# Performance work log

Measured on AMD Instinct MI355X. Metric: run time of the kernel, lower is better.

Reference implementation:

```python
import jax, jax.numpy as jnp
import numpy as np

TARGET_KAPPA = 1.0 / 61.0
EPS = 1e-10

# --- antisymmetric expansion: 35 independent components (i<j<k) -> (7,7,7) ---
_combos = np.array([(i, j, k) for i in range(7) for j in range(i + 1, 7) for k in range(j + 1, 7)])  # (35,3)
_perm_specs = [((0, 1, 2), 1.0), ((0, 2, 1), -1.0), ((1, 0, 2), -1.0), ((1, 2, 0), 1.0), ((2, 0, 1), 1.0), ((2, 1, 0), -1.0)]
_I = jnp.array(np.concatenate([_combos[:, p[0]] for p, _ in _perm_specs]))
_J = jnp.array(np.concatenate([_combos[:, p[1]] for p, _ in _perm_specs]))
_K = jnp.array(np.concatenate([_combos[:, p[2]] for p, _ in _perm_specs]))
_S = jnp.array(np.concatenate([np.full(35, s, dtype=np.float32) for _, s in _perm_specs]))


def expand_to_antisymmetric(v35):
    # v35: (35,) -> antisymmetric (7,7,7)
    vals = jnp.tile(v35, 6) * _S.astype(v35.dtype)
    return jnp.zeros((7, 7, 7), v35.dtype).at[_I, _J, _K].set(vals)


def _phi_single(xi, W1, b1, W2, b2):
    # xi: (7,) -> antisymmetric 3-form (7,7,7)
    h = jnp.tanh(xi @ W1 + b1)          # (H,)
    v35 = h @ W2 + b2                    # (35,)
    return expand_to_antisymmetric(v35)


def setup_inputs() -> dict:
    key = jax.random.key(0)
    k1, k2, k3 = jax.random.split(key, 3)
    B, H = 32768, 512
    x = jax.random.normal(k1, (B, 7), dtype=jnp.float32)
    W1 = jax.random.normal(k2, (7, H), dtype=jnp.float32) * 0.3
    b1 = jnp.zeros((H,), dtype=jnp.float32)
    W2 = jax.random.normal(k3, (H, 35), dtype=jnp.float32) * 0.05
    b2 = jnp.zeros((35,), dtype=jnp.float32)
    return {"x": x, "W1": W1, "b1": b1, "W2": W2, "b2": b2}


def reference(x, W1, b1, W2, b2):
    f = lambda xi: _phi_single(xi, W1, b1, W2, b2)
    # Jacobian replaces the 35 looped autograd.grad calls: (B,7,7,7,7), last axis = d/dx_l
    jac = jax.vmap(jax.jacfwd(f))(x)
    d_phi = jnp.moveaxis(jac, -1, 1)  # (B, 7(deriv), 7, 7, 7), matching torch layout
    torsion_sq = jnp.sum(d_phi ** 2, axis=(1, 2, 3, 4))  # (B,)
    torsion_norm = jnp.sqrt(torsion_sq + EPS)
    loss = jnp.mean((torsion_norm - TARGET_KAPPA) ** 2)
    return loss, jnp.mean(torsion_norm)
```

## Files before the change

### kernel.cpp

```cpp
#include <hip/hip_runtime.h>
#include <hip/hip_bf16.h>
#include <math.h>

typedef __attribute__((ext_vector_type(8)))  short bf16x8;
typedef __attribute__((ext_vector_type(16))) float f32x16;
typedef unsigned int u32;

#define KAPPA (1.0f/61.0f)
#define NBLK 512

__device__ __forceinline__ unsigned short f2bf(float f) {
    u32 x = __float_as_uint(f);
    x += 0x7fffu + ((x >> 16) & 1u);
    return (unsigned short)(x >> 16);
}
__device__ __forceinline__ float fast_rcp(float v) {
#if __has_builtin(__builtin_amdgcn_rcpf)
    return __builtin_amdgcn_rcpf(v);
#else
    return 1.0f / v;
#endif
}
__device__ __forceinline__ u32 pack_bf16(float lo, float hi) {
    __hip_bfloat162 p = __float22bfloat162_rn(make_float2(lo, hi));
    return *reinterpret_cast<u32*>(&p);
}

__global__ void build_v(const float* __restrict__ W1, const float* __restrict__ W2,
                        const float* __restrict__ b1,
                        bf16x8* __restrict__ V, bf16x8* __restrict__ Wt) {
    int t = blockIdx.x * blockDim.x + threadIdx.x;
    if (t < 16384) {
        int lane = t & 63, ptile = (t >> 6) & 7, kkg = t >> 9;
        int p  = ptile * 32 + (lane & 31);
        int hb = kkg * 16 + (lane >> 5) * 8;
        bool valid = (p < 245);
        int l7 = valid ? p / 35 : 0;
        int c  = valid ? p - l7 * 35 : 0;
        bf16x8 v;
#pragma unroll
        for (int i = 0; i < 8; ++i) {
            int h = hb + i;
            v[i] = valid ? (short)f2bf(W1[l7 * 512 + h] * W2[h * 35 + c]) : (short)0;
        }
        V[t] = v;
    } else if (t < 16384 + 1024) {
        int f = t - 16384;
        int lane = f & 63, htile = f >> 6;
        int h = htile * 32 + (lane & 31);
        bf16x8 v;
#pragma unroll
        for (int i = 0; i < 8; ++i) v[i] = 0;
        if (lane < 32) {
#pragma unroll
            for (int l = 0; l < 7; ++l) v[l] = (short)f2bf(W1[l * 512 + h]);
            v[7] = (short)f2bf(b1[h]);
        }
        Wt[f] = v;
    }
}

__global__ __launch_bounds__(256, 3)
void torsion_main(const float* __restrict__ x,
                  const bf16x8* __restrict__ V, const bf16x8* __restrict__ Wt,
                  float* __restrict__ partials) {
    __shared__ __align__(16) u32 Gb[2][8][64 * 4];
    __shared__ float red[4][2][32];

    const int tid  = threadIdx.x;
    const int lane = tid & 63;
    const int w    = tid >> 6;
    const int blk  = blockIdx.x;
    const int rt   = w & 1;
    const int ht   = w >> 1;

    bf16x8 xf;
#pragma unroll
    for (int i = 0; i < 8; ++i) xf[i] = 0;
    if (lane < 32) {
        const float* xp = x + ((size_t)blk * 64 + rt * 32 + lane) * 7;
#pragma unroll
        for (int l = 0; l < 7; ++l) xf[l] = (short)f2bf(xp[l]);
        xf[7] = (short)f2bf(1.0f);
    }

    f32x16 acc[2][2];
#pragma unroll
    for (int pt = 0; pt < 2; ++pt)
#pragma unroll
        for (int r2 = 0; r2 < 2; ++r2)
#pragma unroll
            for (int e = 0; e < 16; ++e) acc[pt][r2][e] = 0.0f;

    auto pre_pack = [&](int c, u32 d[8]) {
        bf16x8 wf = Wt[(c * 2 + ht) * 64 + lane];
        f32x16 p;
#pragma unroll
        for (int e = 0; e < 16; ++e) p[e] = 0.0f;
        p = __builtin_amdgcn_mfma_f32_32x32x16_bf16(wf, xf, p, 0, 0, 0);
#pragma unroll
        for (int j = 0; j < 8; ++j) {
            float g0, g1;
            {
                float t0 = __expf(-2.0f * fabsf(p[2 * j]));
                float r0 = fast_rcp(1.0f + t0);
                g0 = 4.0f * t0 * r0 * r0;
                float t1 = __expf(-2.0f * fabsf(p[2 * j + 1]));
                float r1 = fast_rcp(1.0f + t1);
                g1 = 4.0f * t1 * r1 * r1;
            }
            d[j] = pack_bf16(g0, g1);
        }
    };
    auto store_g = [&](int buf, const u32 d[8]) {
        const int f0  = (2 * ht) * 2 + rt;
        const int f1  = f0 + 2;
        const int col = lane & 31;
        const int hw2 = (lane >> 5) << 1;
        *reinterpret_cast<uint2*>(&Gb[buf][f0][(col      ) * 4 + hw2]) = make_uint2(d[0], d[1]);
        *reinterpret_cast<uint2*>(&Gb[buf][f0][(col + 32 ) * 4 + hw2]) = make_uint2(d[2], d[3]);
        *reinterpret_cast<uint2*>(&Gb[buf][f1][(col      ) * 4 + hw2]) = make_uint2(d[4], d[5]);
        *reinterpret_cast<uint2*>(&Gb[buf][f1][(col + 32 ) * 4 + hw2]) = make_uint2(d[6], d[7]);
    };

    {
        u32 d[8];
        pre_pack(0, d);
        store_g(0, d);
    }
    __syncthreads();

    for (int c = 0; c < 8; ++c) {
        const int buf = c & 1;
        u32 dn[8];
        if (c < 7) pre_pack(c + 1, dn);
#pragma unroll
        for (int ks = 0; ks < 4; ++ks) {
            bf16x8 g0 = *reinterpret_cast<const bf16x8*>(&Gb[buf][ks * 2 + 0][lane * 4]);
            bf16x8 g1 = *reinterpret_cast<const bf16x8*>(&Gb[buf][ks * 2 + 1][lane * 4]);
            const int fb = ((c * 4 + ks) * 8 + 2 * w) * 64 + lane;
            bf16x8 va = V[fb];
            bf16x8 vb = V[fb + 64];
            acc[0][0] = __builtin_amdgcn_mfma_f32_32x32x16_bf16(va, g0, acc[0][0], 0, 0, 0);
            acc[0][1] = __builtin_amdgcn_mfma_f32_32x32x16_bf16(va, g1, acc[0][1], 0, 0, 0);
            acc[1][0] = __builtin_amdgcn_mfma_f32_32x32x16_bf16(vb, g0, acc[1][0], 0, 0, 0);
            acc[1][1] = __builtin_amdgcn_mfma_f32_32x32x16_bf16(vb, g1, acc[1][1], 0, 0, 0);
        }
        if (c < 7) store_g(buf ^ 1, dn);
        __syncthreads();
    }

#pragma unroll
    for (int r2 = 0; r2 < 2; ++r2) {
        float s = 0.0f;
#pragma unroll
        for (int pt = 0; pt < 2; ++pt)
#pragma unroll
            for (int e = 0; e < 16; ++e) s += acc[pt][r2][e] * acc[pt][r2][e];
        s += __shfl_xor(s, 32);
        if (lane < 32) red[w][r2][lane] = s;
    }
    __syncthreads();

    if (tid < 64) {
        const int li = tid & 31, rr = tid >> 5;
        float q = 6.0f * (red[0][rr][li] + red[1][rr][li] + red[2][rr][li] + red[3][rr][li]);
        float n = sqrtf(q + 1e-10f);
        float d = n - KAPPA;
        float a = d * d, b = n;
#pragma unroll
        for (int m = 1; m <= 32; m <<= 1) {
            a += __shfl_xor(a, m);
            b += __shfl_xor(b, m);
        }
        if (tid == 0) {
            partials[blk]        = a;
            partials[NBLK + blk] = b;
        }
    }
}

__global__ void finalize_k(const float* __restrict__ partials, float* __restrict__ out) {
    __shared__ float sl[256], sn[256];
    int tid = threadIdx.x;
    sl[tid] = partials[tid] + partials[tid + 256];
    sn[tid] = partials[NBLK + tid] + partials[NBLK + tid + 256];
    __syncthreads();
    for (int st = 128; st > 0; st >>= 1) {
        if (tid < st) { sl[tid] += sl[tid + st]; sn[tid] += sn[tid + st]; }
        __syncthreads();
    }
    if (tid == 0) {
        out[0] = sl[0] / 32768.0f;
        out[1] = sn[0] / 32768.0f;
    }
}

extern "C" void kernel_launch(void* const* d_in, const int* in_sizes, int n_in,
                              void* d_out, int out_size, void* d_ws, size_t ws_size,
                              hipStream_t stream) {
    const float* x  = (const float*)d_in[0];
    const float* W1 = (const float*)d_in[1];
    const float* b1 = (const float*)d_in[2];
    const float* W2 = (const float*)d_in[3];

    bf16x8* V        = (bf16x8*)d_ws;
    bf16x8* Wt       = V + 16384;
    float*  partials = (float*)(Wt + 1024);

    build_v<<<68, 256, 0, stream>>>(W1, W2, b1, V, Wt);
    torsion_main<<<NBLK, 256, 0, stream>>>(x, V, Wt, partials);
    finalize_k<<<1, 256, 0, stream>>>(partials, (float*)d_out);
}
```

Before: 27.69 us.

## Split block work across 8 waves with halved per-wave MFMA tiles

Doubles the block to 512 threads (8 waves). Each wave now owns one 32-sample sub-tile and one pair of 32-row output tiles instead of two. The hidden dimension is processed in 4 chunks of 128 rather than 8 chunks of 64, with a larger shared G buffer, and s_setprio is raised around the MFMA loop. The intent is more latency hiding per CU and fewer accumulator registers per wave. In exchange, each V fragment is now loaded by two waves, so global/L2 V traffic doubles, and barriers span twice as many waves.

```diff
diff --git a/kernel.cpp b/kernel.cpp
--- a/kernel.cpp
+++ b/kernel.cpp
@@ -60,111 +60,104 @@
     }
 }
 
-__global__ __launch_bounds__(256, 3)
+__global__ __launch_bounds__(512, 4)
 void torsion_main(const float* __restrict__ x,
                   const bf16x8* __restrict__ V, const bf16x8* __restrict__ Wt,
                   float* __restrict__ partials) {
-    __shared__ __align__(16) u32 Gb[2][8][64 * 4];
+    __shared__ __align__(16) u32 Gb[2][16][64 * 4];
     __shared__ float red[4][2][32];
 
     const int tid  = threadIdx.x;
     const int lane = tid & 63;
     const int w    = tid >> 6;
+    const int st   = w & 1;
+    const int pp   = w >> 1;
     const int blk  = blockIdx.x;
-    const int rt   = w & 1;
-    const int ht   = w >> 1;
 
     bf16x8 xf;
 #pragma unroll
     for (int i = 0; i < 8; ++i) xf[i] = 0;
     if (lane < 32) {
-        const float* xp = x + ((size_t)blk * 64 + rt * 32 + lane) * 7;
+        const float* xp = x + ((size_t)blk * 64 + st * 32 + lane) * 7;
 #pragma unroll
         for (int l = 0; l < 7; ++l) xf[l] = (short)f2bf(xp[l]);
         xf[7] = (short)f2bf(1.0f);
     }
 
-    f32x16 acc[2][2];
+    f32x16 acc[2];
 #pragma unroll
     for (int pt = 0; pt < 2; ++pt)
 #pragma unroll
-        for (int r2 = 0; r2 < 2; ++r2)
-#pragma unroll
-            for (int e = 0; e < 16; ++e) acc[pt][r2][e] = 0.0f;
+        for (int e = 0; e < 16; ++e) acc[pt][e] = 0.0f;
 
     auto pre_pack = [&](int c, u32 d[8]) {
-        bf16x8 wf = Wt[(c * 2 + ht) * 64 + lane];
+        bf16x8 wf = Wt[(c * 4 + pp) * 64 + lane];
         f32x16 p;
 #pragma unroll
         for (int e = 0; e < 16; ++e) p[e] = 0.0f;
         p = __builtin_amdgcn_mfma_f32_32x32x16_bf16(wf, xf, p, 0, 0, 0);
 #pragma unroll
         for (int j = 0; j < 8; ++j) {
-            float g0, g1;
-            {
-                float t0 = __expf(-2.0f * fabsf(p[2 * j]));
-                float r0 = fast_rcp(1.0f + t0);
-                g0 = 4.0f * t0 * r0 * r0;
-                float t1 = __expf(-2.0f * fabsf(p[2 * j + 1]));
-                float r1 = fast_rcp(1.0f + t1);
-                g1 = 4.0f * t1 * r1 * r1;
-            }
+            float t0 = __expf(-2.0f * fabsf(p[2 * j]));
+            float r0 = fast_rcp(1.0f + t0);
+            float g0 = 4.0f * t0 * r0 * r0;
+            float t1 = __expf(-2.0f * fabsf(p[2 * j + 1]));
+            float r1 = fast_rcp(1.0f + t1);
+            float g1 = 4.0f * t1 * r1 * r1;
             d[j] = pack_bf16(g0, g1);
         }
     };
     auto store_g = [&](int buf, const u32 d[8]) {
-        const int f0  = (2 * ht) * 2 + rt;
+        const int f0  = 4 * pp + st;
         const int f1  = f0 + 2;
         const int col = lane & 31;
         const int hw2 = (lane >> 5) << 1;
-        *reinterpret_cast<uint2*>(&Gb[buf][f0][(col      ) * 4 + hw2]) = make_uint2(d[0], d[1]);
-        *reinterpret_cast<uint2*>(&Gb[buf][f0][(col + 32 ) * 4 + hw2]) = make_uint2(d[2], d[3]);
-        *reinterpret_cast<uint2*>(&Gb[buf][f1][(col      ) * 4 + hw2]) = make_uint2(d[4], d[5]);
-        *reinterpret_cast<uint2*>(&Gb[buf][f1][(col + 32 ) * 4 + hw2]) = make_uint2(d[6], d[7]);
+        *reinterpret_cast<uint2*>(&Gb[buf][f0][(col     ) * 4 + hw2]) = make_uint2(d[0], d[1]);
+        *reinterpret_cast<uint2*>(&Gb[buf][f0][(col + 32) * 4 + hw2]) = make_uint2(d[2], d[3]);
+        *reinterpret_cast<uint2*>(&Gb[buf][f1][(col     ) * 4 + hw2]) = make_uint2(d[4], d[5]);
+        *reinterpret_cast<uint2*>(&Gb[buf][f1][(col + 32) * 4 + hw2]) = make_uint2(d[6], d[7]);
     };
 
     {
-        u32 d[8];
-        pre_pack(0, d);
-        store_g(0, d);
+        u32 d0[8];
+        pre_pack(0, d0);
+        store_g(0, d0);
     }
     __syncthreads();
 
-    for (int c = 0; c < 8; ++c) {
+    for (int c = 0; c < 4; ++c) {
         const int buf = c & 1;
         u32 dn[8];
-        if (c < 7) pre_pack(c + 1, dn);
-#pragma unroll
-        for (int ks = 0; ks < 4; ++ks) {
-            bf16x8 g0 = *reinterpret_cast<const bf16x8*>(&Gb[buf][ks * 2 + 0][lane * 4]);
-            bf16x8 g1 = *reinterpret_cast<const bf16x8*>(&Gb[buf][ks * 2 + 1][lane * 4]);
-            const int fb = ((c * 4 + ks) * 8 + 2 * w) * 64 + lane;
+        if (c < 3) pre_pack(c + 1, dn);
+        __builtin_amdgcn_s_setprio(1);
+#pragma unroll
+        for (int ks = 0; ks < 8; ++ks) {
+            bf16x8 g = *reinterpret_cast<const bf16x8*>(&Gb[buf][ks * 2 + st][lane * 4]);
+            const int fb = ((c * 8 + ks) * 8 + 2 * pp) * 64 + lane;
             bf16x8 va = V[fb];
             bf16x8 vb = V[fb + 64];
-            acc[0][0] = __builtin_amdgcn_mfma_f32_32x32x16_bf16(va, g0, acc[0][0], 0, 0, 0);
-            acc[0][1] = __builtin_amdgcn_mfma_f32_32x32x16_bf16(va, g1, acc[0][1], 0, 0, 0);
-            acc[1][0] = __builtin_amdgcn_mfma_f32_32x32x16_bf16(vb, g0, acc[1][0], 0, 0, 0);
-            acc[1][1] = __builtin_amdgcn_mfma_f32_32x32x16_bf16(vb, g1, acc[1][1], 0, 0, 0);
-        }
-        if (c < 7) store_g(buf ^ 1, dn);
+            acc[0] = __builtin_amdgcn_mfma_f32_32x32x16_bf16(va, g, acc[0], 0, 0, 0);
+            acc[1] = __builtin_amdgcn_mfma_f32_32x32x16_bf16(vb, g, acc[1], 0, 0, 0);
+        }
+        __builtin_amdgcn_s_setprio(0);
+        if (c < 3) store_g(buf ^ 1, dn);
         __syncthreads();
     }
 
-#pragma unroll
-    for (int r2 = 0; r2 < 2; ++r2) {
+    {
         float s = 0.0f;
 #pragma unroll
         for (int pt = 0; pt < 2; ++pt)
 #pragma unroll
-            for (int e = 0; e < 16; ++e) s += acc[pt][r2][e] * acc[pt][r2][e];
+            for (int e = 0; e < 16; ++e) s += acc[pt][e] * acc[pt][e];
         s += __shfl_xor(s, 32);
-        if (lane < 32) red[w][r2][lane] = s;
+        if (lane < 32) red[pp][st][lane] = s;
     }
     __syncthreads();
 
     if (tid < 64) {
-        const int li = tid & 31, rr = tid >> 5;
-        float q = 6.0f * (red[0][rr][li] + red[1][rr][li] + red[2][rr][li] + red[3][rr][li]);
+        const int col = tid & 31, ss = tid >> 5;
+        float q = 6.0f * (red[0][ss][col] + red[1][ss][col] + red[2][ss][col] + red[3][ss][col]);
         float n = sqrtf(q + 1e-10f);
         float d = n - KAPPA;
         float a = d * d, b = n;
@@ -209,6 +202,6 @@
     float*  partials = (float*)(Wt + 1024);
 
     build_v<<<68, 256, 0, stream>>>(W1, W2, b1, V, Wt);
-    torsion_main<<<NBLK, 256, 0, stream>>>(x, V, Wt, partials);
+    torsion_main<<<NBLK, 512, 0, stream>>>(x, V, Wt, partials);
     finalize_k<<<1, 256, 0, stream>>>(partials, (float*)d_out);
 }
```

New measurement: 28.96 us. 4.6% more time.
